# Kernel tuning notes

Measured on AMD Instinct MI355X. Metric: run time of the kernel, lower is better.

## Reference

```python
import jax, jax.numpy as jnp
import numpy as np

B, IN, OUT, E, CTX, DEMO = 32768, 512, 128, 16, 256, 16
HID = IN // 2
GATE_IN = CTX + IN + DEMO  # 784


def setup_inputs() -> dict:
    key = jax.random.key(0)
    ks = jax.random.split(key, 9)
    inp = {
        'x': jax.random.normal(ks[0], (B, IN), dtype=jnp.float32),
        'u': jax.random.normal(ks[1], (B, CTX), dtype=jnp.float32),
        'd': jax.random.normal(ks[2], (B, DEMO), dtype=jnp.float32),
        # gate Linear(GATE_IN -> E)
        'gate_W': jax.random.normal(ks[3], (E, GATE_IN), dtype=jnp.float32) * 0.02,
        'gate_b': jnp.zeros((E,), dtype=jnp.float32),
        # per-expert MLP: Linear(IN->HID), ReLU, Linear(HID->OUT); stacked over experts
        'W1': jax.random.normal(ks[4], (E, HID, IN), dtype=jnp.float32) * 0.02,
        'b1': jnp.zeros((E, HID), dtype=jnp.float32),
        'W2': jax.random.normal(ks[5], (E, OUT, HID), dtype=jnp.float32) * 0.02,
        'b2': jnp.zeros((E, OUT), dtype=jnp.float32),
    }
    return inp


def reference(x, u, d, gate_W, gate_b, W1, b1, W2, b2):
    # gate input = cat([u, x, d], dim=1)  -> [B, GATE_IN]
    g_in = jnp.concatenate([u, x, d], axis=1)
    gate_logits = g_in @ gate_W.T + gate_b            # [B, E]
    weights = jax.nn.softmax(gate_logits, axis=1)     # [B, E]
    # all-expert MLP as batched GEMMs
    h = jax.nn.relu(jnp.einsum('bi,ehi->beh', x, W1) + b1[None])   # [B, E, HID]
    expert_outputs = jnp.einsum('beh,eoh->beo', h, W2) + b2[None]  # [B, E, OUT]
    # mixture_mode == 'logits': weighted sum over experts
    out = jnp.einsum('be,beo->bo', weights, expert_outputs)        # [B, OUT]
    return out
```

## Files before the change

### kernel.cpp

```cpp
#include <hip/hip_runtime.h>

#define B_    32768
#define IN_   512
#define HID_  256
#define OUT_  128
#define E_    16
#define CTX_  256
#define DEMO_ 16
#define GIN_  784

typedef __attribute__((ext_vector_type(8))) short short8;
typedef __attribute__((ext_vector_type(4))) float floatx4;

__device__ __forceinline__ short f2bf(float x){
  unsigned u = __builtin_bit_cast(unsigned, x);
  u += 0x7FFFu + ((u >> 16) & 1u);
  return (short)(u >> 16);
}

__device__ __forceinline__ void load_lds16(const short* g, short* l){
  __builtin_amdgcn_global_load_lds((const __attribute__((address_space(1))) void*)g,
                                   (__attribute__((address_space(3))) void*)l,
                                   16, 0, 0);
}

__device__ __forceinline__ void stage128x64(short* lds, const short* g, int gpitch, int tid){
  const int wvv = tid >> 6, ln = tid & 63;
  const int cb = ln & 7, rsub = ln >> 3;
  #pragma unroll
  for (int i = 0; i < 4; ++i){
    const int r0  = (wvv*4 + i)*8;
    const int row = r0 + rsub;
    const short* gp = g + (size_t)row*gpitch + ((cb ^ rsub) << 3);
    load_lds16(gp, lds + r0*64);
  }
}

__global__ void convert_kernel(const float* __restrict__ x, const float* __restrict__ w1,
                               const float* __restrict__ w2, short* __restrict__ xb,
                               short* __restrict__ w1b, short* __restrict__ w2b){
  const int N1 = B_*IN_, N2 = E_*HID_*IN_, N3 = E_*OUT_*HID_;
  const int total4 = (N1 + N2 + N3) >> 2;
  for (int i = blockIdx.x*blockDim.x + threadIdx.x; i < total4; i += gridDim.x*blockDim.x){
    int e4 = i << 2;
    const float* src; short* dst; int off;
    if (e4 < N1)            { src = x;  dst = xb;  off = e4; }
    else if (e4 < N1 + N2)  { src = w1; dst = w1b; off = e4 - N1; }
    else                    { src = w2; dst = w2b; off = e4 - (N1 + N2); }
    float4 v = *(const float4*)(src + off);
    *(short4*)(dst + off) = make_short4(f2bf(v.x), f2bf(v.y), f2bf(v.z), f2bf(v.w));
  }
}

__global__ void gate_kernel(const float* __restrict__ u, const float* __restrict__ x,
                            const float* __restrict__ d, const float* __restrict__ gW,
                            const float* __restrict__ gb, float* __restrict__ wout){
  const int lane = threadIdx.x & 63;
  const int row  = blockIdx.x*4 + (threadIdx.x >> 6);
  float acc[E_];
  #pragma unroll
  for (int e = 0; e < E_; ++e) acc[e] = 0.f;
  #pragma unroll
  for (int t = 0; t < 12; ++t){
    const int i = t*64 + lane;
    const float v = (t < 4) ? u[row*CTX_ + i] : x[row*IN_ + (i - 256)];
    #pragma unroll
    for (int e = 0; e < E_; ++e) acc[e] += v * gW[e*GIN_ + i];
  }
  if (lane < DEMO_){
    const float v = d[row*DEMO_ + lane];
    #pragma unroll
    for (int e = 0; e < E_; ++e) acc[e] += v * gW[e*GIN_ + 768 + lane];
  }
  #pragma unroll
  for (int e = 0; e < E_; ++e){
    #pragma unroll
    for (int m = 32; m >= 1; m >>= 1) acc[e] += __shfl_xor(acc[e], m);
  }
  if (lane == 0){
    float mx = -1e30f;
    #pragma unroll
    for (int e = 0; e < E_; ++e){ acc[e] += gb[e]; mx = fmaxf(mx, acc[e]); }
    float s = 0.f;
    #pragma unroll
    for (int e = 0; e < E_; ++e){ acc[e] = __expf(acc[e] - mx); s += acc[e]; }
    const float inv = 1.f / s;
    #pragma unroll
    for (int e = 0; e < E_; ++e) wout[row*E_ + e] = acc[e] * inv;
  }
}

__global__ __launch_bounds__(256, 2)
void moe_kernel(const short* __restrict__ xb, const short* __restrict__ w1b,
                const short* __restrict__ w2b, const float* __restrict__ gatew,
                const float* __restrict__ b1g, const float* __restrict__ b2g,
                float* __restrict__ out){
  __shared__ alignas(16) char smem[51200];
  short* s_x = (short*)smem;
  short* s_h = (short*)smem;
  short* s_w = (short*)(smem + 34816);

  const int tid  = threadIdx.x;
  const int wv   = tid >> 6;
  const int lane = tid & 63;
  const int l15  = lane & 15;
  const int hi2  = lane >> 4;
  const int m_off = (wv >> 1) * 64;
  const int n_off = (wv & 1) * 64;
  const int blk_m0 = blockIdx.x * 128;
  const int eg = blockIdx.y;

  floatx4 oacc[4][4];
  #pragma unroll
  for (int a = 0; a < 4; ++a)
    #pragma unroll
    for (int b = 0; b < 4; ++b) oacc[a][b] = floatx4{0.f, 0.f, 0.f, 0.f};

  if (eg == 0){
    #pragma unroll 1
    for (int e = 0; e < E_; ++e){
      float b2v[4];
      #pragma unroll
      for (int nt = 0; nt < 4; ++nt) b2v[nt] = b2g[e*OUT_ + n_off + nt*16 + l15];
      #pragma unroll
      for (int mt = 0; mt < 4; ++mt){
        #pragma unroll
        for (int r = 0; r < 4; ++r){
          const float wgt = gatew[(blk_m0 + m_off + mt*16 + hi2*4 + r)*E_ + e];
          #pragma unroll
          for (int nt = 0; nt < 4; ++nt) oacc[mt][nt][r] += wgt * b2v[nt];
        }
      }
    }
  }

  #pragma unroll 1
  for (int ei = 0; ei < 8; ++ei){
    const int e = eg*8 + ei;
    #pragma unroll 1
    for (int half = 0; half < 2; ++half){
      floatx4 g1[4][4];
      #pragma unroll
      for (int a = 0; a < 4; ++a)
        #pragma unroll
        for (int b = 0; b < 4; ++b) g1[a][b] = floatx4{0.f, 0.f, 0.f, 0.f};

      const short* w1base = w1b + (size_t)(e*HID_ + half*128) * IN_;
      #pragma unroll 1
      for (int kc = 0; kc < 8; ++kc){
        stage128x64(s_x, xb + (size_t)blk_m0*IN_ + kc*64, IN_, tid);
        stage128x64(s_w, w1base + kc*64, IN_, tid);
        __syncthreads();
        #pragma unroll
        for (int ks = 0; ks < 2; ++ks){
          const int kb = ks*4 + hi2;
          const int sw = (kb ^ (l15 & 7)) << 3;
          short8 af[4], bf[4];
          #pragma unroll
          for (int mt = 0; mt < 4; ++mt)
            af[mt] = *(const short8*)&s_x[(m_off + mt*16 + l15)*64 + sw];
          #pragma unroll
          for (int nt = 0; nt < 4; ++nt)
            bf[nt] = *(const short8*)&s_w[(n_off + nt*16 + l15)*64 + sw];
          #pragma unroll
          for (int mt = 0; mt < 4; ++mt)
            #pragma unroll
            for (int nt = 0; nt < 4; ++nt)
              g1[mt][nt] = __builtin_amdgcn_mfma_f32_16x16x32_bf16(af[mt], bf[nt], g1[mt][nt], 0, 0, 0);
        }
        __syncthreads();
      }

      const short* w2base = w2b + (size_t)e*OUT_*HID_ + half*128;
      stage128x64(s_w, w2base, HID_, tid);

      {
        float b1v[4];
        #pragma unroll
        for (int nt = 0; nt < 4; ++nt)
          b1v[nt] = b1g[e*HID_ + half*128 + n_off + nt*16 + l15];
        #pragma unroll
        for (int mt = 0; mt < 4; ++mt){
          #pragma unroll
          for (int r = 0; r < 4; ++r){
            const int m = m_off + mt*16 + hi2*4 + r;
            const float wgt = gatew[(blk_m0 + m)*E_ + e];
            #pragma unroll
            for (int nt = 0; nt < 4; ++nt){
              float hv = g1[mt][nt][r] + b1v[nt];
              hv = fmaxf(hv, 0.f) * wgt;
              s_h[m*136 + n_off + nt*16 + l15] = f2bf(hv);
            }
          }
        }
      }
      __syncthreads();

      #pragma unroll 1
      for (int kc2 = 0; kc2 < 2; ++kc2){
        #pragma unroll
        for (int ks = 0; ks < 2; ++ks){
          const int kb = ks*4 + hi2;
          const int kk = kc2*64 + (kb << 3);
          const int sw = (kb ^ (l15 & 7)) << 3;
          short8 af[4], bf[4];
          #pragma unroll
          for (int mt = 0; mt < 4; ++mt)
            af[mt] = *(const short8*)&s_h[(m_off + mt*16 + l15)*136 + kk];
          #pragma unroll
          for (int nt = 0; nt < 4; ++nt)
            bf[nt] = *(const short8*)&s_w[(n_off + nt*16 + l15)*64 + sw];
          #pragma unroll
          for (int mt = 0; mt < 4; ++mt)
            #pragma unroll
            for (int nt = 0; nt < 4; ++nt)
              oacc[mt][nt] = __builtin_amdgcn_mfma_f32_16x16x32_bf16(af[mt], bf[nt], oacc[mt][nt], 0, 0, 0);
        }
        __syncthreads();
        if (kc2 == 0){
          stage128x64(s_w, w2base + 64, HID_, tid);
          __syncthreads();
        }
      }
    }
  }

  #pragma unroll
  for (int mt = 0; mt < 4; ++mt)
    #pragma unroll
    for (int nt = 0; nt < 4; ++nt)
      #pragma unroll
      for (int r = 0; r < 4; ++r)
        atomicAdd(&out[(size_t)(blk_m0 + m_off + mt*16 + hi2*4 + r)*OUT_ + n_off + nt*16 + l15],
                  oacc[mt][nt][r]);
}

extern "C" void kernel_launch(void* const* d_in, const int* in_sizes, int n_in,
                              void* d_out, int out_size, void* d_ws, size_t ws_size,
                              hipStream_t stream){
  const float* x  = (const float*)d_in[0];
  const float* u  = (const float*)d_in[1];
  const float* dd = (const float*)d_in[2];
  const float* gW = (const float*)d_in[3];
  const float* gb = (const float*)d_in[4];
  const float* W1 = (const float*)d_in[5];
  const float* b1 = (const float*)d_in[6];
  const float* W2 = (const float*)d_in[7];
  const float* b2 = (const float*)d_in[8];
  float* out = (float*)d_out;

  short* xb  = (short*)d_ws;
  short* w1b = xb  + (size_t)B_*IN_;
  short* w2b = w1b + (size_t)E_*HID_*IN_;
  float* gw  = (float*)(w2b + (size_t)E_*OUT_*HID_);

  hipMemsetAsync(d_out, 0, (size_t)B_*OUT_*sizeof(float), stream);
  hipLaunchKernelGGL(convert_kernel, dim3(4096), dim3(256), 0, stream, x, W1, W2, xb, w1b, w2b);
  hipLaunchKernelGGL(gate_kernel, dim3(B_/4), dim3(256), 0, stream, u, x, dd, gW, gb, gw);
  hipLaunchKernelGGL(moe_kernel, dim3(B_/128, 2), dim3(256), 0, stream, xb, w1b, w2b, gw, b1, b2, out);
  (void)in_sizes; (void)n_in; (void)out_size; (void)ws_size;
}
```

Baseline: 413.8 us.

## Use MFMA for gate GEMM, transpose expert GEMM1, split experts over four groups

The gate kernel is rewritten to compute logits with bf16 MFMA over 16-row tiles, reading the already-converted bf16 x. The softmax is done with shuffles across 16 lanes. In the MoE kernel the first GEMM is transposed (W1 as A operand, x as B), which allows packed short4 writes of the hidden tile, and s_w1/s_w2 get separate LDS regions. The expert grid dimension grows from 2 to 4 groups to raise parallelism, at the cost of twice as many atomic adds to the output. Gate precision drops from fp32 to bf16 inputs.

```diff
diff --git a/kernel.cpp b/kernel.cpp
--- a/kernel.cpp
+++ b/kernel.cpp
@@ -16,6 +16,13 @@
   unsigned u = __builtin_bit_cast(unsigned, x);
   u += 0x7FFFu + ((u >> 16) & 1u);
   return (short)(u >> 16);
+}
+
+__device__ __forceinline__ short8 pack8(float4 a, float4 b){
+  short8 r;
+  r[0]=f2bf(a.x); r[1]=f2bf(a.y); r[2]=f2bf(a.z); r[3]=f2bf(a.w);
+  r[4]=f2bf(b.x); r[5]=f2bf(b.y); r[6]=f2bf(b.z); r[7]=f2bf(b.w);
+  return r;
 }
 
 __device__ __forceinline__ void load_lds16(const short* g, short* l){
@@ -52,41 +59,59 @@
   }
 }
 
-__global__ void gate_kernel(const float* __restrict__ u, const float* __restrict__ x,
-                            const float* __restrict__ d, const float* __restrict__ gW,
-                            const float* __restrict__ gb, float* __restrict__ wout){
-  const int lane = threadIdx.x & 63;
-  const int row  = blockIdx.x*4 + (threadIdx.x >> 6);
-  float acc[E_];
-  #pragma unroll
-  for (int e = 0; e < E_; ++e) acc[e] = 0.f;
-  #pragma unroll
-  for (int t = 0; t < 12; ++t){
-    const int i = t*64 + lane;
-    const float v = (t < 4) ? u[row*CTX_ + i] : x[row*IN_ + (i - 256)];
-    #pragma unroll
-    for (int e = 0; e < E_; ++e) acc[e] += v * gW[e*GIN_ + i];
-  }
-  if (lane < DEMO_){
-    const float v = d[row*DEMO_ + lane];
-    #pragma unroll
-    for (int e = 0; e < E_; ++e) acc[e] += v * gW[e*GIN_ + 768 + lane];
-  }
-  #pragma unroll
-  for (int e = 0; e < E_; ++e){
-    #pragma unroll
-    for (int m = 32; m >= 1; m >>= 1) acc[e] += __shfl_xor(acc[e], m);
-  }
-  if (lane == 0){
-    float mx = -1e30f;
-    #pragma unroll
-    for (int e = 0; e < E_; ++e){ acc[e] += gb[e]; mx = fmaxf(mx, acc[e]); }
-    float s = 0.f;
-    #pragma unroll
-    for (int e = 0; e < E_; ++e){ acc[e] = __expf(acc[e] - mx); s += acc[e]; }
-    const float inv = 1.f / s;
-    #pragma unroll
-    for (int e = 0; e < E_; ++e) wout[row*E_ + e] = acc[e] * inv;
+__global__ __launch_bounds__(256)
+void gate_kernel(const float* __restrict__ u, const short* __restrict__ xb,
+                 const float* __restrict__ d, const float* __restrict__ gW,
+                 const float* __restrict__ gb, float* __restrict__ wout){
+  const int tid  = threadIdx.x;
+  const int wave = tid >> 6, lane = tid & 63;
+  const int l15  = lane & 15, quad = lane >> 4;
+  const int row0 = blockIdx.x*64 + wave*16;
+  const int rA   = row0 + l15;
+  const int kq   = quad*8;
+
+  floatx4 acc  = {0.f,0.f,0.f,0.f};
+  floatx4 acc2 = {0.f,0.f,0.f,0.f};
+
+  #pragma unroll
+  for (int t = 0; t < 8; ++t){
+    const float4 a0 = *(const float4*)&u[(size_t)rA*CTX_ + t*32 + kq];
+    const float4 a1 = *(const float4*)&u[(size_t)rA*CTX_ + t*32 + kq + 4];
+    const float4 b0 = *(const float4*)&gW[(size_t)l15*GIN_ + t*32 + kq];
+    const float4 b1 = *(const float4*)&gW[(size_t)l15*GIN_ + t*32 + kq + 4];
+    acc = __builtin_amdgcn_mfma_f32_16x16x32_bf16(pack8(a0,a1), pack8(b0,b1), acc, 0,0,0);
+  }
+  #pragma unroll
+  for (int t = 0; t < 16; ++t){
+    const short8 af = *(const short8*)&xb[(size_t)rA*IN_ + t*32 + kq];
+    const float4 b0 = *(const float4*)&gW[(size_t)l15*GIN_ + 256 + t*32 + kq];
+    const float4 b1 = *(const float4*)&gW[(size_t)l15*GIN_ + 256 + t*32 + kq + 4];
+    acc2 = __builtin_amdgcn_mfma_f32_16x16x32_bf16(af, pack8(b0,b1), acc2, 0,0,0);
+  }
+  {
+    short8 af = {0,0,0,0,0,0,0,0}, bf = {0,0,0,0,0,0,0,0};
+    if (quad < 2){
+      const float4 a0 = *(const float4*)&d[(size_t)rA*DEMO_ + kq];
+      const float4 a1 = *(const float4*)&d[(size_t)rA*DEMO_ + kq + 4];
+      const float4 b0 = *(const float4*)&gW[(size_t)l15*GIN_ + 768 + kq];
+      const float4 b1 = *(const float4*)&gW[(size_t)l15*GIN_ + 768 + kq + 4];
+      af = pack8(a0,a1); bf = pack8(b0,b1);
+    }
+    acc = __builtin_amdgcn_mfma_f32_16x16x32_bf16(af, bf, acc, 0,0,0);
+  }
+
+  const float bias = gb[l15];
+  #pragma unroll
+  for (int r = 0; r < 4; ++r){
+    float v = acc[r] + acc2[r] + bias;
+    float m = v;
+    #pragma unroll
+    for (int s = 1; s <= 8; s <<= 1) m = fmaxf(m, __shfl_xor(m, s));
+    const float p = __expf(v - m);
+    float ssum = p;
+    #pragma unroll
+    for (int s = 1; s <= 8; s <<= 1) ssum += __shfl_xor(ssum, s);
+    wout[(size_t)(row0 + quad*4 + r)*E_ + l15] = p / ssum;
   }
 }
 
@@ -96,17 +121,20 @@
                 const float* __restrict__ b1g, const float* __restrict__ b2g,
                 float* __restrict__ out){
   __shared__ alignas(16) char smem[51200];
-  short* s_x = (short*)smem;
-  short* s_h = (short*)smem;
-  short* s_w = (short*)(smem + 34816);
+  short* s_x  = (short*)smem;
+  short* s_w1 = (short*)(smem + 16384);
+  short* s_h  = (short*)smem;
+  short* s_w2 = (short*)(smem + 34816);
 
   const int tid  = threadIdx.x;
   const int wv   = tid >> 6;
   const int lane = tid & 63;
   const int l15  = lane & 15;
   const int hi2  = lane >> 4;
-  const int m_off = (wv >> 1) * 64;
-  const int n_off = (wv & 1) * 64;
+  const int h_off  = (wv >> 1) * 64;
+  const int mb_off = (wv & 1) * 64;
+  const int m_off  = (wv >> 1) * 64;
+  const int o_off  = (wv & 1) * 64;
   const int blk_m0 = blockIdx.x * 128;
   const int eg = blockIdx.y;
 
@@ -114,19 +142,19 @@
   #pragma unroll
   for (int a = 0; a < 4; ++a)
     #pragma unroll
-    for (int b = 0; b < 4; ++b) oacc[a][b] = floatx4{0.f, 0.f, 0.f, 0.f};
+    for (int b = 0; b < 4; ++b) oacc[a][b] = floatx4{0.f,0.f,0.f,0.f};
 
   if (eg == 0){
     #pragma unroll 1
     for (int e = 0; e < E_; ++e){
       float b2v[4];
       #pragma unroll
-      for (int nt = 0; nt < 4; ++nt) b2v[nt] = b2g[e*OUT_ + n_off + nt*16 + l15];
+      for (int nt = 0; nt < 4; ++nt) b2v[nt] = b2g[e*OUT_ + o_off + nt*16 + l15];
       #pragma unroll
       for (int mt = 0; mt < 4; ++mt){
         #pragma unroll
         for (int r = 0; r < 4; ++r){
-          const float wgt = gatew[(blk_m0 + m_off + mt*16 + hi2*4 + r)*E_ + e];
+          const float wgt = gatew[(size_t)(blk_m0 + m_off + mt*16 + hi2*4 + r)*E_ + e];
           #pragma unroll
           for (int nt = 0; nt < 4; ++nt) oacc[mt][nt][r] += wgt * b2v[nt];
         }
@@ -135,21 +163,21 @@
   }
 
   #pragma unroll 1
-  for (int ei = 0; ei < 8; ++ei){
-    const int e = eg*8 + ei;
+  for (int ei = 0; ei < 4; ++ei){
+    const int e = eg*4 + ei;
     #pragma unroll 1
     for (int half = 0; half < 2; ++half){
       floatx4 g1[4][4];
       #pragma unroll
       for (int a = 0; a < 4; ++a)
         #pragma unroll
-        for (int b = 0; b < 4; ++b) g1[a][b] = floatx4{0.f, 0.f, 0.f, 0.f};
+        for (int b = 0; b < 4; ++b) g1[a][b] = floatx4{0.f,0.f,0.f,0.f};
 
       const short* w1base = w1b + (size_t)(e*HID_ + half*128) * IN_;
       #pragma unroll 1
       for (int kc = 0; kc < 8; ++kc){
-        stage128x64(s_x, xb + (size_t)blk_m0*IN_ + kc*64, IN_, tid);
-        stage128x64(s_w, w1base + kc*64, IN_, tid);
+        stage128x64(s_x,  xb + (size_t)blk_m0*IN_ + kc*64, IN_, tid);
+        stage128x64(s_w1, w1base + kc*64, IN_, tid);
         __syncthreads();
         #pragma unroll
         for (int ks = 0; ks < 2; ++ks){
@@ -157,40 +185,44 @@
           const int sw = (kb ^ (l15 & 7)) << 3;
           short8 af[4], bf[4];
           #pragma unroll
+          for (int ht = 0; ht < 4; ++ht)
+            af[ht] = *(const short8*)&s_w1[(h_off + ht*16 + l15)*64 + sw];
+          #pragma unroll
           for (int mt = 0; mt < 4; ++mt)
-            af[mt] = *(const short8*)&s_x[(m_off + mt*16 + l15)*64 + sw];
-          #pragma unroll
-          for (int nt = 0; nt < 4; ++nt)
-            bf[nt] = *(const short8*)&s_w[(n_off + nt*16 + l15)*64 + sw];
-          #pragma unroll
-          for (int mt = 0; mt < 4; ++mt)
+            bf[mt] = *(const short8*)&s_x[(mb_off + mt*16 + l15)*64 + sw];
+          #pragma unroll
+          for (int ht = 0; ht < 4; ++ht)
             #pragma unroll
-            for (int nt = 0; nt < 4; ++nt)
-              g1[mt][nt] = __builtin_amdgcn_mfma_f32_16x16x32_bf16(af[mt], bf[nt], g1[mt][nt], 0, 0, 0);
+            for (int mt = 0; mt < 4; ++mt)
+              g1[ht][mt] = __builtin_amdgcn_mfma_f32_16x16x32_bf16(af[ht], bf[mt], g1[ht][mt], 0,0,0);
         }
         __syncthreads();
       }
 
       const short* w2base = w2b + (size_t)e*OUT_*HID_ + half*128;
-      stage128x64(s_w, w2base, HID_, tid);
+      stage128x64(s_w2, w2base, HID_, tid);
 
       {
-        float b1v[4];
-        #pragma unroll
-        for (int nt = 0; nt < 4; ++nt)
-          b1v[nt] = b1g[e*HID_ + half*128 + n_off + nt*16 + l15];
-        #pragma unroll
-        for (int mt = 0; mt < 4; ++mt){
-          #pragma unroll
-          for (int r = 0; r < 4; ++r){
-            const int m = m_off + mt*16 + hi2*4 + r;
-            const float wgt = gatew[(blk_m0 + m)*E_ + e];
-            #pragma unroll
-            for (int nt = 0; nt < 4; ++nt){
-              float hv = g1[mt][nt][r] + b1v[nt];
-              hv = fmaxf(hv, 0.f) * wgt;
-              s_h[m*136 + n_off + nt*16 + l15] = f2bf(hv);
-            }
+        float4 b1v[4];
+        #pragma unroll
+        for (int ht = 0; ht < 4; ++ht)
+          b1v[ht] = *(const float4*)&b1g[e*HID_ + half*128 + h_off + ht*16 + hi2*4];
+        float wgt[4];
+        #pragma unroll
+        for (int mt = 0; mt < 4; ++mt)
+          wgt[mt] = gatew[(size_t)(blk_m0 + mb_off + mt*16 + l15)*E_ + e];
+        #pragma unroll
+        for (int ht = 0; ht < 4; ++ht){
+          const float b1r[4] = {b1v[ht].x, b1v[ht].y, b1v[ht].z, b1v[ht].w};
+          #pragma unroll
+          for (int mt = 0; mt < 4; ++mt){
+            short4 pk;
+            float v0 = fmaxf(g1[ht][mt][0] + b1r[0], 0.f) * wgt[mt];
+            float v1 = fmaxf(g1[ht][mt][1] + b1r[1], 0.f) * wgt[mt];
+            float v2 = fmaxf(g1[ht][mt][2] + b1r[2], 0.f) * wgt[mt];
+            float v3 = fmaxf(g1[ht][mt][3] + b1r[3], 0.f) * wgt[mt];
+            pk.x = f2bf(v0); pk.y = f2bf(v1); pk.z = f2bf(v2); pk.w = f2bf(v3);
+            *(short4*)&s_h[(size_t)(mb_off + mt*16 + l15)*136 + h_off + ht*16 + hi2*4] = pk;
           }
         }
       }
@@ -209,16 +241,16 @@
             af[mt] = *(const short8*)&s_h[(m_off + mt*16 + l15)*136 + kk];
           #pragma unroll
           for (int nt = 0; nt < 4; ++nt)
-            bf[nt] = *(const short8*)&s_w[(n_off + nt*16 + l15)*64 + sw];
+            bf[nt] = *(const short8*)&s_w2[(o_off + nt*16 + l15)*64 + sw];
           #pragma unroll
           for (int mt = 0; mt < 4; ++mt)
             #pragma unroll
             for (int nt = 0; nt < 4; ++nt)
-              oacc[mt][nt] = __builtin_amdgcn_mfma_f32_16x16x32_bf16(af[mt], bf[nt], oacc[mt][nt], 0, 0, 0);
+              oacc[mt][nt] = __builtin_amdgcn_mfma_f32_16x16x32_bf16(af[mt], bf[nt], oacc[mt][nt], 0,0,0);
         }
         __syncthreads();
         if (kc2 == 0){
-          stage128x64(s_w, w2base + 64, HID_, tid);
+          stage128x64(s_w2, w2base + 64, HID_, tid);
           __syncthreads();
         }
       }
@@ -231,7 +263,7 @@
     for (int nt = 0; nt < 4; ++nt)
       #pragma unroll
       for (int r = 0; r < 4; ++r)
-        atomicAdd(&out[(size_t)(blk_m0 + m_off + mt*16 + hi2*4 + r)*OUT_ + n_off + nt*16 + l15],
+        atomicAdd(&out[(size_t)(blk_m0 + m_off + mt*16 + hi2*4 + r)*OUT_ + o_off + nt*16 + l15],
                   oacc[mt][nt][r]);
 }
 
@@ -256,7 +288,7 @@
 
   hipMemsetAsync(d_out, 0, (size_t)B_*OUT_*sizeof(float), stream);
   hipLaunchKernelGGL(convert_kernel, dim3(4096), dim3(256), 0, stream, x, W1, W2, xb, w1b, w2b);
-  hipLaunchKernelGGL(gate_kernel, dim3(B_/4), dim3(256), 0, stream, u, x, dd, gW, gb, gw);
-  hipLaunchKernelGGL(moe_kernel, dim3(B_/128, 2), dim3(256), 0, stream, xb, w1b, w2b, gw, b1, b2, out);
+  hipLaunchKernelGGL(gate_kernel, dim3(B_/64), dim3(256), 0, stream, u, xb, dd, gW, gb, gw);
+  hipLaunchKernelGGL(moe_kernel, dim3(B_/128, 4), dim3(256), 0, stream, xb, w1b, w2b, gw, b1, b2, out);
   (void)in_sizes; (void)n_in; (void)out_size; (void)ws_size;
 }
```

After: 383.4 us. -7.3%, faster.

## Fuse gate softmax into MoE kernel and restructure per-expert GEMM tiling

Applied to the files above, without the earlier changes.

Removes the separate gate kernel and computes the gating logits with bf16 MFMA inside the MoE kernel, then keeps the softmax weights in LDS. Each 512-thread block now owns 64 rows across all 16 experts. The full x tile stays resident in LDS while W1 and W2 fragments are read directly from global memory, and the hidden activations stay in registers between the two GEMMs. Output is reduced across warps in LDS and written once, which removes the memset and the atomics. This trades LDS staging of weights for direct global (L2) weight reads, and the gate now runs in bf16 precision instead of fp32.

```diff
diff --git a/kernel.cpp b/kernel.cpp
--- a/kernel.cpp
+++ b/kernel.cpp
@@ -18,22 +18,17 @@
   return (short)(u >> 16);
 }
 
+__device__ __forceinline__ short8 pack8(float4 a, float4 b){
+  short8 r;
+  r[0]=f2bf(a.x); r[1]=f2bf(a.y); r[2]=f2bf(a.z); r[3]=f2bf(a.w);
+  r[4]=f2bf(b.x); r[5]=f2bf(b.y); r[6]=f2bf(b.z); r[7]=f2bf(b.w);
+  return r;
+}
+
 __device__ __forceinline__ void load_lds16(const short* g, short* l){
   __builtin_amdgcn_global_load_lds((const __attribute__((address_space(1))) void*)g,
                                    (__attribute__((address_space(3))) void*)l,
                                    16, 0, 0);
-}
-
-__device__ __forceinline__ void stage128x64(short* lds, const short* g, int gpitch, int tid){
-  const int wvv = tid >> 6, ln = tid & 63;
-  const int cb = ln & 7, rsub = ln >> 3;
-  #pragma unroll
-  for (int i = 0; i < 4; ++i){
-    const int r0  = (wvv*4 + i)*8;
-    const int row = r0 + rsub;
-    const short* gp = g + (size_t)row*gpitch + ((cb ^ rsub) << 3);
-    load_lds16(gp, lds + r0*64);
-  }
 }
 
 __global__ void convert_kernel(const float* __restrict__ x, const float* __restrict__ w1,
@@ -52,187 +47,221 @@
   }
 }
 
-__global__ void gate_kernel(const float* __restrict__ u, const float* __restrict__ x,
-                            const float* __restrict__ d, const float* __restrict__ gW,
-                            const float* __restrict__ gb, float* __restrict__ wout){
-  const int lane = threadIdx.x & 63;
-  const int row  = blockIdx.x*4 + (threadIdx.x >> 6);
-  float acc[E_];
-  #pragma unroll
-  for (int e = 0; e < E_; ++e) acc[e] = 0.f;
-  #pragma unroll
-  for (int t = 0; t < 12; ++t){
-    const int i = t*64 + lane;
-    const float v = (t < 4) ? u[row*CTX_ + i] : x[row*IN_ + (i - 256)];
-    #pragma unroll
-    for (int e = 0; e < E_; ++e) acc[e] += v * gW[e*GIN_ + i];
-  }
-  if (lane < DEMO_){
-    const float v = d[row*DEMO_ + lane];
-    #pragma unroll
-    for (int e = 0; e < E_; ++e) acc[e] += v * gW[e*GIN_ + 768 + lane];
-  }
-  #pragma unroll
-  for (int e = 0; e < E_; ++e){
-    #pragma unroll
-    for (int m = 32; m >= 1; m >>= 1) acc[e] += __shfl_xor(acc[e], m);
-  }
-  if (lane == 0){
-    float mx = -1e30f;
-    #pragma unroll
-    for (int e = 0; e < E_; ++e){ acc[e] += gb[e]; mx = fmaxf(mx, acc[e]); }
-    float s = 0.f;
-    #pragma unroll
-    for (int e = 0; e < E_; ++e){ acc[e] = __expf(acc[e] - mx); s += acc[e]; }
-    const float inv = 1.f / s;
-    #pragma unroll
-    for (int e = 0; e < E_; ++e) wout[row*E_ + e] = acc[e] * inv;
-  }
-}
-
-__global__ __launch_bounds__(256, 2)
+__global__ __launch_bounds__(512, 2)
 void moe_kernel(const short* __restrict__ xb, const short* __restrict__ w1b,
-                const short* __restrict__ w2b, const float* __restrict__ gatew,
+                const short* __restrict__ w2b,
+                const float* __restrict__ u, const float* __restrict__ dd,
+                const float* __restrict__ gWf, const float* __restrict__ gbf,
                 const float* __restrict__ b1g, const float* __restrict__ b2g,
                 float* __restrict__ out){
-  __shared__ alignas(16) char smem[51200];
-  short* s_x = (short*)smem;
-  short* s_h = (short*)smem;
-  short* s_w = (short*)(smem + 34816);
+  __shared__ alignas(16) short s_x[64*512];
 
   const int tid  = threadIdx.x;
   const int wv   = tid >> 6;
   const int lane = tid & 63;
   const int l15  = lane & 15;
   const int hi2  = lane >> 4;
-  const int m_off = (wv >> 1) * 64;
-  const int n_off = (wv & 1) * 64;
-  const int blk_m0 = blockIdx.x * 128;
-  const int eg = blockIdx.y;
-
-  floatx4 oacc[4][4];
+  const int m_g  = wv & 1;
+  const int h_g  = wv >> 1;
+  const int blk_m0 = blockIdx.x * 64;
+
+  float* sg = (float*)s_x;
+
+  if (wv < 4){
+    const int mrow = blk_m0 + wv*16 + l15;
+    floatx4 ga = {0.f,0.f,0.f,0.f};
+    #pragma unroll
+    for (int t = 0; t < 8; ++t){
+      const int k = t*32 + hi2*8;
+      short8 bfr = pack8(*(const float4*)&u[(size_t)mrow*CTX_ + k],
+                         *(const float4*)&u[(size_t)mrow*CTX_ + k + 4]);
+      short8 afr = pack8(*(const float4*)&gWf[(size_t)l15*GIN_ + k],
+                         *(const float4*)&gWf[(size_t)l15*GIN_ + k + 4]);
+      ga = __builtin_amdgcn_mfma_f32_16x16x32_bf16(afr, bfr, ga, 0,0,0);
+    }
+    #pragma unroll
+    for (int t = 0; t < 16; ++t){
+      const int k = t*32 + hi2*8;
+      short8 bfr = *(const short8*)&xb[(size_t)mrow*IN_ + k];
+      short8 afr = pack8(*(const float4*)&gWf[(size_t)l15*GIN_ + 256 + k],
+                         *(const float4*)&gWf[(size_t)l15*GIN_ + 256 + k + 4]);
+      ga = __builtin_amdgcn_mfma_f32_16x16x32_bf16(afr, bfr, ga, 0,0,0);
+    }
+    {
+      short8 afr = {0,0,0,0,0,0,0,0}, bfr = {0,0,0,0,0,0,0,0};
+      if (hi2 < 2){
+        bfr = pack8(*(const float4*)&dd[(size_t)mrow*DEMO_ + hi2*8],
+                    *(const float4*)&dd[(size_t)mrow*DEMO_ + hi2*8 + 4]);
+        afr = pack8(*(const float4*)&gWf[(size_t)l15*GIN_ + 768 + hi2*8],
+                    *(const float4*)&gWf[(size_t)l15*GIN_ + 768 + hi2*8 + 4]);
+      }
+      ga = __builtin_amdgcn_mfma_f32_16x16x32_bf16(afr, bfr, ga, 0,0,0);
+    }
+    float v[4];
+    #pragma unroll
+    for (int r = 0; r < 4; ++r) v[r] = ga[r] + gbf[hi2*4 + r];
+    float mx = fmaxf(fmaxf(v[0],v[1]), fmaxf(v[2],v[3]));
+    mx = fmaxf(mx, __shfl_xor(mx, 16));
+    mx = fmaxf(mx, __shfl_xor(mx, 32));
+    float p[4], s = 0.f;
+    #pragma unroll
+    for (int r = 0; r < 4; ++r){ p[r] = __expf(v[r]-mx); s += p[r]; }
+    s += __shfl_xor(s, 16);
+    s += __shfl_xor(s, 32);
+    const float inv = 1.f / s;
+    #pragma unroll
+    for (int r = 0; r < 4; ++r) sg[(wv*16 + l15)*17 + hi2*4 + r] = p[r]*inv;
+  }
+  __syncthreads();
+
+  floatx4 oacc[2][8];
   #pragma unroll
-  for (int a = 0; a < 4; ++a)
-    #pragma unroll
-    for (int b = 0; b < 4; ++b) oacc[a][b] = floatx4{0.f, 0.f, 0.f, 0.f};
-
-  if (eg == 0){
+  for (int mt = 0; mt < 2; ++mt)
+    #pragma unroll
+    for (int ot = 0; ot < 8; ++ot) oacc[mt][ot] = floatx4{0.f,0.f,0.f,0.f};
+  if (h_g == 0){
     #pragma unroll 1
     for (int e = 0; e < E_; ++e){
-      float b2v[4];
-      #pragma unroll
-      for (int nt = 0; nt < 4; ++nt) b2v[nt] = b2g[e*OUT_ + n_off + nt*16 + l15];
-      #pragma unroll
-      for (int mt = 0; mt < 4; ++mt){
+      float b2v[8];
+      #pragma unroll
+      for (int ot = 0; ot < 8; ++ot) b2v[ot] = b2g[e*OUT_ + ot*16 + l15];
+      #pragma unroll
+      for (int mt = 0; mt < 2; ++mt)
         #pragma unroll
         for (int r = 0; r < 4; ++r){
-          const float wgt = gatew[(blk_m0 + m_off + mt*16 + hi2*4 + r)*E_ + e];
+          const float wg = sg[(m_g*32 + mt*16 + hi2*4 + r)*17 + e];
           #pragma unroll
-          for (int nt = 0; nt < 4; ++nt) oacc[mt][nt][r] += wgt * b2v[nt];
+          for (int ot = 0; ot < 8; ++ot) oacc[mt][ot][r] += wg*b2v[ot];
         }
+    }
+  }
+  float w_my[2][16];
+  #pragma unroll
+  for (int mt = 0; mt < 2; ++mt)
+    #pragma unroll
+    for (int e = 0; e < E_; ++e)
+      w_my[mt][e] = sg[(m_g*32 + mt*16 + l15)*17 + e];
+  __syncthreads();
+
+  #pragma unroll
+  for (int i = 0; i < 8; ++i){
+    const int row = wv + i*8;
+    const int cb  = (lane & 56) | ((lane ^ row) & 7);
+    load_lds16(&xb[(size_t)(blk_m0 + row)*IN_ + cb*8], s_x + row*512);
+  }
+  __syncthreads();
+
+  #pragma unroll 1
+  for (int e = 0; e < E_; ++e){
+    floatx4 g1[2][4];
+    #pragma unroll
+    for (int ht = 0; ht < 4; ++ht){
+      const float4 bv = *(const float4*)&b1g[e*HID_ + h_g*64 + ht*16 + hi2*4];
+      g1[0][ht] = floatx4{bv.x, bv.y, bv.z, bv.w};
+      g1[1][ht] = g1[0][ht];
+    }
+    const short* w1e = w1b + ((size_t)e*HID_ + h_g*64) * IN_;
+    #pragma unroll
+    for (int ks = 0; ks < 16; ++ks){
+      short8 af[4], bf[2];
+      #pragma unroll
+      for (int ht = 0; ht < 4; ++ht)
+        af[ht] = *(const short8*)&w1e[(size_t)(ht*16 + l15)*IN_ + ks*32 + hi2*8];
+      #pragma unroll
+      for (int mt = 0; mt < 2; ++mt){
+        const int m   = m_g*32 + mt*16 + l15;
+        const int cbl = ks*4 + hi2;
+        const int phys = (cbl & ~7) | ((cbl ^ m) & 7);
+        bf[mt] = *(const short8*)&s_x[m*512 + phys*8];
       }
-    }
-  }
-
-  #pragma unroll 1
-  for (int ei = 0; ei < 8; ++ei){
-    const int e = eg*8 + ei;
-    #pragma unroll 1
-    for (int half = 0; half < 2; ++half){
-      floatx4 g1[4][4];
-      #pragma unroll
-      for (int a = 0; a < 4; ++a)
-        #pragma unroll
-        for (int b = 0; b < 4; ++b) g1[a][b] = floatx4{0.f, 0.f, 0.f, 0.f};
-
-      const short* w1base = w1b + (size_t)(e*HID_ + half*128) * IN_;
-      #pragma unroll 1
-      for (int kc = 0; kc < 8; ++kc){
-        stage128x64(s_x, xb + (size_t)blk_m0*IN_ + kc*64, IN_, tid);
-        stage128x64(s_w, w1base + kc*64, IN_, tid);
-        __syncthreads();
-        #pragma unroll
-        for (int ks = 0; ks < 2; ++ks){
-          const int kb = ks*4 + hi2;
-          const int sw = (kb ^ (l15 & 7)) << 3;
-          short8 af[4], bf[4];
-          #pragma unroll
-          for (int mt = 0; mt < 4; ++mt)
-            af[mt] = *(const short8*)&s_x[(m_off + mt*16 + l15)*64 + sw];
-          #pragma unroll
-          for (int nt = 0; nt < 4; ++nt)
-            bf[nt] = *(const short8*)&s_w[(n_off + nt*16 + l15)*64 + sw];
-          #pragma unroll
-          for (int mt = 0; mt < 4; ++mt)
-            #pragma unroll
-            for (int nt = 0; nt < 4; ++nt)
-              g1[mt][nt] = __builtin_amdgcn_mfma_f32_16x16x32_bf16(af[mt], bf[nt], g1[mt][nt], 0, 0, 0);
+      #pragma unroll
+      for (int mt = 0; mt < 2; ++mt)
+        #pragma unroll
+        for (int ht = 0; ht < 4; ++ht)
+          g1[mt][ht] = __builtin_amdgcn_mfma_f32_16x16x32_bf16(af[ht], bf[mt], g1[mt][ht], 0,0,0);
+    }
+
+    short8 a2[2][2];
+    #pragma unroll
+    for (int mt = 0; mt < 2; ++mt){
+      const float wg = w_my[mt][e];
+      short pk[16];
+      #pragma unroll
+      for (int ht = 0; ht < 4; ++ht)
+        #pragma unroll
+        for (int r = 0; r < 4; ++r)
+          pk[ht*4 + r] = f2bf(fmaxf(g1[mt][ht][r], 0.f) * wg);
+      #pragma unroll
+      for (int ks = 0; ks < 2; ++ks)
+        #pragma unroll
+        for (int j = 0; j < 8; ++j)
+          a2[ks][mt][j] = pk[ks*8 + j];
+    }
+
+    const short* w2e = w2b + (size_t)e*OUT_*HID_ + h_g*64;
+    #pragma unroll
+    for (int ot = 0; ot < 8; ++ot){
+      #pragma unroll
+      for (int ks = 0; ks < 2; ++ks){
+        const short* p = &w2e[(size_t)(ot*16 + l15)*HID_ + ks*32 + hi2*4];
+        const short4 lo = *(const short4*)p;
+        const short4 hi = *(const short4*)(p + 16);
+        short8 bfr;
+        bfr[0]=lo.x; bfr[1]=lo.y; bfr[2]=lo.z; bfr[3]=lo.w;
+        bfr[4]=hi.x; bfr[5]=hi.y; bfr[6]=hi.z; bfr[7]=hi.w;
+        #pragma unroll
+        for (int mt = 0; mt < 2; ++mt)
+          oacc[mt][ot] = __builtin_amdgcn_mfma_f32_16x16x32_bf16(a2[ks][mt], bfr, oacc[mt][ot], 0,0,0);
+      }
+    }
+    __builtin_amdgcn_s_barrier();
+  }
+
+  __syncthreads();
+  float* red = (float*)s_x;
+  if (h_g >= 2){
+    const int s = (h_g - 2)*2 + m_g;
+    #pragma unroll
+    for (int mt = 0; mt < 2; ++mt)
+      #pragma unroll
+      for (int ot = 0; ot < 8; ++ot)
+        #pragma unroll
+        for (int r = 0; r < 4; ++r)
+          red[s*4096 + (mt*16 + hi2*4 + r)*128 + ot*16 + l15] = oacc[mt][ot][r];
+  }
+  __syncthreads();
+  if (h_g < 2){
+    const int s = h_g*2 + m_g;
+    #pragma unroll
+    for (int mt = 0; mt < 2; ++mt)
+      #pragma unroll
+      for (int ot = 0; ot < 8; ++ot)
+        #pragma unroll
+        for (int r = 0; r < 4; ++r)
+          oacc[mt][ot][r] += red[s*4096 + (mt*16 + hi2*4 + r)*128 + ot*16 + l15];
+  }
+  __syncthreads();
+  if (h_g == 1){
+    #pragma unroll
+    for (int mt = 0; mt < 2; ++mt)
+      #pragma unroll
+      for (int ot = 0; ot < 8; ++ot)
+        #pragma unroll
+        for (int r = 0; r < 4; ++r)
+          red[m_g*4096 + (mt*16 + hi2*4 + r)*128 + ot*16 + l15] = oacc[mt][ot][r];
+  }
+  __syncthreads();
+  if (h_g == 0){
+    #pragma unroll
+    for (int mt = 0; mt < 2; ++mt)
+      #pragma unroll
+      for (int ot = 0; ot < 8; ++ot)
+        #pragma unroll
+        for (int r = 0; r < 4; ++r){
+          const float v = oacc[mt][ot][r] + red[m_g*4096 + (mt*16 + hi2*4 + r)*128 + ot*16 + l15];
+          out[(size_t)(blk_m0 + m_g*32 + mt*16 + hi2*4 + r)*OUT_ + ot*16 + l15] = v;
         }
-        __syncthreads();
-      }
-
-      const short* w2base = w2b + (size_t)e*OUT_*HID_ + half*128;
-      stage128x64(s_w, w2base, HID_, tid);
-
-      {
-        float b1v[4];
-        #pragma unroll
-        for (int nt = 0; nt < 4; ++nt)
-          b1v[nt] = b1g[e*HID_ + half*128 + n_off + nt*16 + l15];
-        #pragma unroll
-        for (int mt = 0; mt < 4; ++mt){
-          #pragma unroll
-          for (int r = 0; r < 4; ++r){
-            const int m = m_off + mt*16 + hi2*4 + r;
-            const float wgt = gatew[(blk_m0 + m)*E_ + e];
-            #pragma unroll
-            for (int nt = 0; nt < 4; ++nt){
-              float hv = g1[mt][nt][r] + b1v[nt];
-              hv = fmaxf(hv, 0.f) * wgt;
-              s_h[m*136 + n_off + nt*16 + l15] = f2bf(hv);
-            }
-          }
-        }
-      }
-      __syncthreads();
-
-      #pragma unroll 1
-      for (int kc2 = 0; kc2 < 2; ++kc2){
-        #pragma unroll
-        for (int ks = 0; ks < 2; ++ks){
-          const int kb = ks*4 + hi2;
-          const int kk = kc2*64 + (kb << 3);
-          const int sw = (kb ^ (l15 & 7)) << 3;
-          short8 af[4], bf[4];
-          #pragma unroll
-          for (int mt = 0; mt < 4; ++mt)
-            af[mt] = *(const short8*)&s_h[(m_off + mt*16 + l15)*136 + kk];
-          #pragma unroll
-          for (int nt = 0; nt < 4; ++nt)
-            bf[nt] = *(const short8*)&s_w[(n_off + nt*16 + l15)*64 + sw];
-          #pragma unroll
-          for (int mt = 0; mt < 4; ++mt)
-            #pragma unroll
-            for (int nt = 0; nt < 4; ++nt)
-              oacc[mt][nt] = __builtin_amdgcn_mfma_f32_16x16x32_bf16(af[mt], bf[nt], oacc[mt][nt], 0, 0, 0);
-        }
-        __syncthreads();
-        if (kc2 == 0){
-          stage128x64(s_w, w2base + 64, HID_, tid);
-          __syncthreads();
-        }
-      }
-    }
-  }
-
-  #pragma unroll
-  for (int mt = 0; mt < 4; ++mt)
-    #pragma unroll
-    for (int nt = 0; nt < 4; ++nt)
-      #pragma unroll
-      for (int r = 0; r < 4; ++r)
-        atomicAdd(&out[(size_t)(blk_m0 + m_off + mt*16 + hi2*4 + r)*OUT_ + n_off + nt*16 + l15],
-                  oacc[mt][nt][r]);
+  }
 }
 
 extern "C" void kernel_launch(void* const* d_in, const int* in_sizes, int n_in,
@@ -252,11 +281,9 @@
   short* xb  = (short*)d_ws;
   short* w1b = xb  + (size_t)B_*IN_;
   short* w2b = w1b + (size_t)E_*HID_*IN_;
-  float* gw  = (float*)(w2b + (size_t)E_*OUT_*HID_);
-
-  hipMemsetAsync(d_out, 0, (size_t)B_*OUT_*sizeof(float), stream);
+
   hipLaunchKernelGGL(convert_kernel, dim3(4096), dim3(256), 0, stream, x, W1, W2, xb, w1b, w2b);
-  hipLaunchKernelGGL(gate_kernel, dim3(B_/4), dim3(256), 0, stream, u, x, dd, gW, gb, gw);
-  hipLaunchKernelGGL(moe_kernel, dim3(B_/128, 2), dim3(256), 0, stream, xb, w1b, w2b, gw, b1, b2, out);
+  hipLaunchKernelGGL(moe_kernel, dim3(B_/64), dim3(512), 0, stream,
+                     xb, w1b, w2b, u, dd, gW, gb, b1, b2, out);
   (void)in_sizes; (void)n_in; (void)out_size; (void)ws_size;
 }
```

Measured after the change: 850.0 us. 105% more time.
